# Performance work log

Hardware: AMD Instinct MI355X
Metric: run time of the kernel (lower is better)

## Reference

```python
import jax, jax.numpy as jnp
import numpy as np

E = 16          # num_expert
CAP = 1024


def setup_inputs() -> dict:
    key = jax.random.key(0)
    k1, k2, k3, k4 = jax.random.split(key, 4)
    B, L, D_in, D_out, S = 2, 4096, 1024, 4096, 512
    inp = jax.random.normal(k1, (B, L, D_in), jnp.float32)
    # counts must sum to B*L; use a balanced assignment (tokens pre-sorted by expert)
    fwd_expert_count = jnp.full((E,), (B * L) // E, dtype=jnp.int32)
    weight = jax.random.normal(k2, (E, D_out, D_in), jnp.float32) * (1.0 / np.sqrt(D_in))
    bias = jax.random.normal(k3, (E, D_out), jnp.float32) * 0.02
    components = jax.random.normal(k4, (E, S, D_out), jnp.float32) * (1.0 / np.sqrt(D_out))
    return {"inp": inp, "fwd_expert_count": fwd_expert_count, "weight": weight,
            "bias": bias, "components": components}


def _forward(inp, fwd_expert_count, weight, bias, components):
    flat = inp.reshape(-1, inp.shape[-1])            # [T, D_in]
    T = flat.shape[0]
    n_exp = fwd_expert_count.shape[0]
    counts = fwd_expert_count.astype(jnp.int32)
    # per-token expert id and position within its expert segment (tokens are
    # contiguous per expert, matching fastmoe's dispatch layout)
    expert_ids = jnp.repeat(jnp.arange(n_exp, dtype=jnp.int32), counts,
                            total_repeat_length=T)                    # [T]
    offsets = jnp.concatenate([jnp.zeros((1,), jnp.int32), jnp.cumsum(counts)])
    pos = jnp.arange(T, dtype=jnp.int32) - offsets[expert_ids]        # [T]
    # scatter tokens into a padded [E, CAP, D_in] buffer (static capacity)
    padded = jnp.zeros((n_exp, CAP, flat.shape[-1]), flat.dtype)
    padded = padded.at[expert_ids, pos].set(flat)
    # grouped expert GEMM: y_e = x_e @ W_e^T + b_e  (padded rows never read back)
    y = jnp.einsum('eci,eoi->eco', padded, weight) + bias[:, None, :]  # [E, CAP, D_out]
    # projection onto components (einsum 'nkd,ksd->nks' in padded layout)
    proj = jnp.einsum('ecd,esd->ecs', y, components)                   # [E, CAP, S]
    # gather real tokens back (the upscale_proj branch in the source is dead code:
    # its result is never used in the returned output)
    out = proj[expert_ids, pos]                                        # [T, S]
    return out.reshape(inp.shape[:-1] + (proj.shape[-1],))


def reference(inp, fwd_expert_count, weight, bias, components):
    return _forward(inp, fwd_expert_count, weight, bias, components)
```

## Files before the change

### kernel.cpp

```cpp
#include <hip/hip_runtime.h>


#define NEXP 16
#define TTOK 8192
#define DIN  1024
#define DOUT 4096
#define SDIM 512
#define LDSS 40

typedef short short8 __attribute__((ext_vector_type(8)));
typedef float floatx4 __attribute__((ext_vector_type(4)));
typedef unsigned short ushort_t;

__device__ __forceinline__ ushort_t f2bf(float f) {
    union { float f; unsigned u; } v; v.f = f;
    unsigned r = v.u + 0x7FFFu + ((v.u >> 16) & 1u);
    return (ushort_t)(r >> 16);
}

#define GLL16(g, l) __builtin_amdgcn_global_load_lds( \
    (const __attribute__((address_space(1))) void*)(g), \
    (__attribute__((address_space(3))) void*)(l), 16, 0, 0)

__global__ __launch_bounds__(256)
void cvt_kernel(const float* __restrict__ src, ushort_t* __restrict__ dst, int n8) {
    const int i = blockIdx.x * 256 + threadIdx.x;
    if (i >= n8) return;
    const float4 a = ((const float4*)src)[2 * i];
    const float4 b = ((const float4*)src)[2 * i + 1];
    short8 o;
    o[0] = (short)f2bf(a.x); o[1] = (short)f2bf(a.y);
    o[2] = (short)f2bf(a.z); o[3] = (short)f2bf(a.w);
    o[4] = (short)f2bf(b.x); o[5] = (short)f2bf(b.y);
    o[6] = (short)f2bf(b.z); o[7] = (short)f2bf(b.w);
    ((short8*)dst)[i] = o;
}

__global__ __launch_bounds__(256, 3)
void gemm1_f(const ushort_t* __restrict__ Xb, const int* __restrict__ counts,
             const ushort_t* __restrict__ Wb, const float* __restrict__ bias,
             ushort_t* __restrict__ Y) {
    __shared__ __align__(16) ushort_t As[128 * 32];
    __shared__ __align__(16) ushort_t Bs[128 * 32];

    const int l = ((blockIdx.x & 7) << 8) | (blockIdx.x >> 3);
    const int e = l >> 7;
    const int r = l & 127;
    const int n_tile = r >> 2, m_tile = r & 3;

    int off = 0;
    for (int i = 0; i < e; ++i) off += counts[i];
    const int cnt = counts[e];

    const int t = threadIdx.x, wave = t >> 6, lane = t & 63;
    const int wm = (wave & 1) << 6, wn = (wave >> 1) << 6;
    const int l15 = lane & 15, quad = lane >> 4;

    const int g = (lane & 3) ^ ((lane >> 3) & 3);
    const int c0 = wave * 2, c1 = wave * 2 + 1;
    const int ar0 = c0 * 16 + (lane >> 2), ar1 = c1 * 16 + (lane >> 2);
    int xr0 = off + (m_tile << 7) + ar0; if (xr0 >= TTOK) xr0 = TTOK - 1;
    int xr1 = off + (m_tile << 7) + ar1; if (xr1 >= TTOK) xr1 = TTOK - 1;
    const ushort_t* gA0 = Xb + (size_t)xr0 * DIN + g * 8;
    const ushort_t* gA1 = Xb + (size_t)xr1 * DIN + g * 8;
    const ushort_t* Wp = Wb + (size_t)e * DOUT * DIN + (size_t)(n_tile << 7) * DIN;
    const ushort_t* gB0 = Wp + (size_t)ar0 * DIN + g * 8;
    const ushort_t* gB1 = Wp + (size_t)ar1 * DIN + g * 8;
    ushort_t* lA0 = As + c0 * 512; ushort_t* lA1 = As + c1 * 512;
    ushort_t* lB0 = Bs + c0 * 512; ushort_t* lB1 = Bs + c1 * 512;

    const int sw = (quad ^ ((l15 >> 1) & 3)) << 3;

    floatx4 acc[4][4] = {};

    for (int k0 = 0; k0 < DIN; k0 += 32) {
        GLL16(gA0, lA0); GLL16(gA1, lA1);
        GLL16(gB0, lB0); GLL16(gB1, lB1);
        gA0 += 32; gA1 += 32; gB0 += 32; gB1 += 32;
        __syncthreads();
        short8 af[4], bfr[4];
        #pragma unroll
        for (int i = 0; i < 4; ++i) {
            af[i]  = *(const short8*)&As[(wm + (i << 4) + l15) * 32 + sw];
            bfr[i] = *(const short8*)&Bs[(wn + (i << 4) + l15) * 32 + sw];
        }
        #pragma unroll
        for (int mi = 0; mi < 4; ++mi)
            #pragma unroll
            for (int ni = 0; ni < 4; ++ni)
                acc[mi][ni] = __builtin_amdgcn_mfma_f32_16x16x32_bf16(
                    af[mi], bfr[ni], acc[mi][ni], 0, 0, 0);
        __syncthreads();
    }

    float bv[4];
    #pragma unroll
    for (int ni = 0; ni < 4; ++ni)
        bv[ni] = bias[e * DOUT + (n_tile << 7) + wn + (ni << 4) + l15];

    #pragma unroll
    for (int mi = 0; mi < 4; ++mi) {
        #pragma unroll
        for (int rg = 0; rg < 4; ++rg) {
            const int trow = (m_tile << 7) + wm + (mi << 4) + (quad << 2) + rg;
            if (trow < cnt) {
                ushort_t* yp = Y + (size_t)(off + trow) * DOUT + (n_tile << 7) + wn;
                #pragma unroll
                for (int ni = 0; ni < 4; ++ni)
                    yp[(ni << 4) + l15] = f2bf(acc[mi][ni][rg] + bv[ni]);
            }
        }
    }
}

__global__ __launch_bounds__(256, 3)
void gemm2_f(const ushort_t* __restrict__ Y, const int* __restrict__ counts,
             const ushort_t* __restrict__ Cb, float* __restrict__ P) {
    __shared__ __align__(16) ushort_t As[128 * 32];
    __shared__ __align__(16) ushort_t Bs[128 * 32];

    const int l = ((blockIdx.x & 7) << 6) | (blockIdx.x >> 3);
    const int e = l >> 5;
    const int r = l & 31;
    const int n_tile = r >> 3;
    const int kh = (r >> 2) & 1;
    const int m_tile = r & 3;

    int off = 0;
    for (int i = 0; i < e; ++i) off += counts[i];
    const int cnt = counts[e];

    const int t = threadIdx.x, wave = t >> 6, lane = t & 63;
    const int wm = (wave & 1) << 6, wn = (wave >> 1) << 6;
    const int l15 = lane & 15, quad = lane >> 4;

    const int g = (lane & 3) ^ ((lane >> 3) & 3);
    const int c0 = wave * 2, c1 = wave * 2 + 1;
    const int ar0 = c0 * 16 + (lane >> 2), ar1 = c1 * 16 + (lane >> 2);
    int yr0 = off + (m_tile << 7) + ar0; if (yr0 >= TTOK) yr0 = TTOK - 1;
    int yr1 = off + (m_tile << 7) + ar1; if (yr1 >= TTOK) yr1 = TTOK - 1;
    const int kbase = kh * 2048;
    const ushort_t* gA0 = Y + (size_t)yr0 * DOUT + kbase + g * 8;
    const ushort_t* gA1 = Y + (size_t)yr1 * DOUT + kbase + g * 8;
    const ushort_t* Cp = Cb + (size_t)e * SDIM * DOUT + (size_t)(n_tile << 7) * DOUT;
    const ushort_t* gB0 = Cp + (size_t)ar0 * DOUT + kbase + g * 8;
    const ushort_t* gB1 = Cp + (size_t)ar1 * DOUT + kbase + g * 8;
    ushort_t* lA0 = As + c0 * 512; ushort_t* lA1 = As + c1 * 512;
    ushort_t* lB0 = Bs + c0 * 512; ushort_t* lB1 = Bs + c1 * 512;

    const int sw = (quad ^ ((l15 >> 1) & 3)) << 3;

    floatx4 acc[4][4] = {};

    for (int it = 0; it < 64; ++it) {
        GLL16(gA0, lA0); GLL16(gA1, lA1);
        GLL16(gB0, lB0); GLL16(gB1, lB1);
        gA0 += 32; gA1 += 32; gB0 += 32; gB1 += 32;
        __syncthreads();
        short8 af[4], bfr[4];
        #pragma unroll
        for (int i = 0; i < 4; ++i) {
            af[i]  = *(const short8*)&As[(wm + (i << 4) + l15) * 32 + sw];
            bfr[i] = *(const short8*)&Bs[(wn + (i << 4) + l15) * 32 + sw];
        }
        #pragma unroll
        for (int mi = 0; mi < 4; ++mi)
            #pragma unroll
            for (int ni = 0; ni < 4; ++ni)
                acc[mi][ni] = __builtin_amdgcn_mfma_f32_16x16x32_bf16(
                    af[mi], bfr[ni], acc[mi][ni], 0, 0, 0);
        __syncthreads();
    }

    float* Pk = P + (size_t)kh * (TTOK * SDIM);
    #pragma unroll
    for (int mi = 0; mi < 4; ++mi) {
        #pragma unroll
        for (int rg = 0; rg < 4; ++rg) {
            const int trow = (m_tile << 7) + wm + (mi << 4) + (quad << 2) + rg;
            if (trow < cnt) {
                float* op = Pk + (size_t)(off + trow) * SDIM + (n_tile << 7) + wn;
                #pragma unroll
                for (int ni = 0; ni < 4; ++ni)
                    op[(ni << 4) + l15] = acc[mi][ni][rg];
            }
        }
    }
}

__global__ __launch_bounds__(256)
void reduce2_kernel(const float* __restrict__ P, float* __restrict__ O) {
    const int i = blockIdx.x * 256 + threadIdx.x;
    const float4 a = ((const float4*)P)[i];
    const float4 b = ((const float4*)(P + (size_t)TTOK * SDIM))[i];
    ((float4*)O)[i] = make_float4(a.x + b.x, a.y + b.y, a.z + b.z, a.w + b.w);
}

__global__ __launch_bounds__(256, 2)
void gemm1_o(const float* __restrict__ X, const int* __restrict__ counts,
             const float* __restrict__ W, const float* __restrict__ bias,
             ushort_t* __restrict__ Y) {
    __shared__ __align__(16) ushort_t As[128 * LDSS];
    __shared__ __align__(16) ushort_t Bs[128 * LDSS];
    const int bid = blockIdx.x;
    const int e = bid >> 7, r_ = bid & 127;
    const int n_tile = r_ >> 2, m_tile = r_ & 3;
    int off = 0;
    for (int i = 0; i < e; ++i) off += counts[i];
    const int cnt = counts[e];
    const int t = threadIdx.x, wave = t >> 6, lane = t & 63;
    const int wm = (wave & 1) << 6, wn = (wave >> 1) << 6;
    const int l15 = lane & 15, quad = lane >> 4;
    const float* Wp = W + (size_t)e * DOUT * DIN + (size_t)(n_tile << 7) * DIN;
    floatx4 acc[4][4] = {};
    const int srow = t >> 3, scol = (t & 7) << 2;
    for (int k0 = 0; k0 < DIN; k0 += 32) {
        #pragma unroll
        for (int p = 0; p < 4; ++p) {
            const int row = srow + (p << 5);
            int grow = off + (m_tile << 7) + row;
            if (grow >= TTOK) grow = 0;
            const float4 v = *(const float4*)(X + (size_t)grow * DIN + k0 + scol);
            unsigned lo = (unsigned)f2bf(v.x) | ((unsigned)f2bf(v.y) << 16);
            unsigned hi = (unsigned)f2bf(v.z) | ((unsigned)f2bf(v.w) << 16);
            *(uint2*)&As[row * LDSS + scol] = make_uint2(lo, hi);
        }
        #pragma unroll
        for (int p = 0; p < 4; ++p) {
            const int row = srow + (p << 5);
            const float4 v = *(const float4*)(Wp + (size_t)row * DIN + k0 + scol);
            unsigned lo = (unsigned)f2bf(v.x) | ((unsigned)f2bf(v.y) << 16);
            unsigned hi = (unsigned)f2bf(v.z) | ((unsigned)f2bf(v.w) << 16);
            *(uint2*)&Bs[row * LDSS + scol] = make_uint2(lo, hi);
        }
        __syncthreads();
        short8 af[4], bfr[4];
        #pragma unroll
        for (int i = 0; i < 4; ++i) {
            af[i]  = *(const short8*)&As[(wm + (i << 4) + l15) * LDSS + (quad << 3)];
            bfr[i] = *(const short8*)&Bs[(wn + (i << 4) + l15) * LDSS + (quad << 3)];
        }
        #pragma unroll
        for (int mi = 0; mi < 4; ++mi)
            #pragma unroll
            for (int ni = 0; ni < 4; ++ni)
                acc[mi][ni] = __builtin_amdgcn_mfma_f32_16x16x32_bf16(
                    af[mi], bfr[ni], acc[mi][ni], 0, 0, 0);
        __syncthreads();
    }
    float bv[4];
    #pragma unroll
    for (int ni = 0; ni < 4; ++ni)
        bv[ni] = bias[e * DOUT + (n_tile << 7) + wn + (ni << 4) + l15];
    #pragma unroll
    for (int mi = 0; mi < 4; ++mi)
        #pragma unroll
        for (int rg = 0; rg < 4; ++rg) {
            const int trow = (m_tile << 7) + wm + (mi << 4) + (quad << 2) + rg;
            if (trow < cnt) {
                ushort_t* yp = Y + (size_t)(off + trow) * DOUT + (n_tile << 7) + wn;
                #pragma unroll
                for (int ni = 0; ni < 4; ++ni)
                    yp[(ni << 4) + l15] = f2bf(acc[mi][ni][rg] + bv[ni]);
            }
        }
}

__global__ __launch_bounds__(256, 2)
void gemm2_o(const ushort_t* __restrict__ Y, const int* __restrict__ counts,
             const float* __restrict__ C, float* __restrict__ O) {
    __shared__ __align__(16) ushort_t As[128 * LDSS];
    __shared__ __align__(16) ushort_t Bs[128 * LDSS];
    const int bid = blockIdx.x;
    const int e = bid >> 4, r_ = bid & 15;
    const int n_tile = r_ >> 2, m_tile = r_ & 3;
    int off = 0;
    for (int i = 0; i < e; ++i) off += counts[i];
    const int cnt = counts[e];
    const int t = threadIdx.x, wave = t >> 6, lane = t & 63;
    const int wm = (wave & 1) << 6, wn = (wave >> 1) << 6;
    const int l15 = lane & 15, quad = lane >> 4;
    const float* Cp = C + (size_t)e * SDIM * DOUT + (size_t)(n_tile << 7) * DOUT;
    floatx4 acc[4][4] = {};
    const int arow = t >> 2, achk = (t & 3) << 3;
    const int srow = t >> 3, scol = (t & 7) << 2;
    for (int k0 = 0; k0 < DOUT; k0 += 32) {
        #pragma unroll
        for (int p = 0; p < 2; ++p) {
            const int row = arow + (p << 6);
            int grow = off + (m_tile << 7) + row;
            if (grow >= TTOK) grow = 0;
            const short8 v = *(const short8*)(Y + (size_t)grow * DOUT + k0 + achk);
            *(short8*)&As[row * LDSS + achk] = v;
        }
        #pragma unroll
        for (int p = 0; p < 4; ++p) {
            const int row = srow + (p << 5);
            const float4 v = *(const float4*)(Cp + (size_t)row * DOUT + k0 + scol);
            unsigned lo = (unsigned)f2bf(v.x) | ((unsigned)f2bf(v.y) << 16);
            unsigned hi = (unsigned)f2bf(v.z) | ((unsigned)f2bf(v.w) << 16);
            *(uint2*)&Bs[row * LDSS + scol] = make_uint2(lo, hi);
        }
        __syncthreads();
        short8 af[4], bfr[4];
        #pragma unroll
        for (int i = 0; i < 4; ++i) {
            af[i]  = *(const short8*)&As[(wm + (i << 4) + l15) * LDSS + (quad << 3)];
            bfr[i] = *(const short8*)&Bs[(wn + (i << 4) + l15) * LDSS + (quad << 3)];
        }
        #pragma unroll
        for (int mi = 0; mi < 4; ++mi)
            #pragma unroll
            for (int ni = 0; ni < 4; ++ni)
                acc[mi][ni] = __builtin_amdgcn_mfma_f32_16x16x32_bf16(
                    af[mi], bfr[ni], acc[mi][ni], 0, 0, 0);
        __syncthreads();
    }
    #pragma unroll
    for (int mi = 0; mi < 4; ++mi)
        #pragma unroll
        for (int rg = 0; rg < 4; ++rg) {
            const int trow = (m_tile << 7) + wm + (mi << 4) + (quad << 2) + rg;
            if (trow < cnt) {
                float* op = O + (size_t)(off + trow) * SDIM + (n_tile << 7) + wn;
                #pragma unroll
                for (int ni = 0; ni < 4; ++ni)
                    op[(ni << 4) + l15] = acc[mi][ni][rg];
            }
        }
}

extern "C" void kernel_launch(void* const* d_in, const int* in_sizes, int n_in,
                              void* d_out, int out_size, void* d_ws, size_t ws_size,
                              hipStream_t stream) {
    const float* X      = (const float*)d_in[0];
    const int*   counts = (const int*)d_in[1];
    const float* W      = (const float*)d_in[2];
    const float* bias   = (const float*)d_in[3];
    const float* comp   = (const float*)d_in[4];
    float* out = (float*)d_out;

    const size_t OFF_XB = 0;
    const size_t OFF_WB = 16777216;
    const size_t OFF_CB = 150994944;
    const size_t OFF_Y  = 218103808;
    const size_t NEED   = 285212672;

    if (ws_size >= NEED) {
        ushort_t* Xb = (ushort_t*)((char*)d_ws + OFF_XB);
        ushort_t* Wb = (ushort_t*)((char*)d_ws + OFF_WB);
        ushort_t* Cb = (ushort_t*)((char*)d_ws + OFF_CB);
        ushort_t* Y  = (ushort_t*)((char*)d_ws + OFF_Y);
        float*    P  = (float*)d_ws;

        cvt_kernel<<<dim3(4096),  dim3(256), 0, stream>>>(X, Xb, 1048576);
        cvt_kernel<<<dim3(32768), dim3(256), 0, stream>>>(W, Wb, 8388608);
        cvt_kernel<<<dim3(16384), dim3(256), 0, stream>>>(comp, Cb, 4194304);
        gemm1_f<<<dim3(2048), dim3(256), 0, stream>>>(Xb, counts, Wb, bias, Y);
        gemm2_f<<<dim3(512),  dim3(256), 0, stream>>>(Y, counts, Cb, P);
        reduce2_kernel<<<dim3(4096), dim3(256), 0, stream>>>(P, out);
    } else {
        ushort_t* Y = (ushort_t*)d_ws;
        gemm1_o<<<dim3(2048), dim3(256), 0, stream>>>(X, counts, W, bias, Y);
        gemm2_o<<<dim3(256),  dim3(256), 0, stream>>>(Y, counts, comp, out);
    }
}
```

Before: 654.6 us.

## Replace bf16 GEMMs with 256x256-tile double-buffered 8-wave pipelined kernel

Replaces the two 128x128, 4-wave, single-buffered grouped GEMMs with one templated 512-thread kernel. It uses 256x256 tiles, BK=64 double-buffered LDS, XOR-swizzled layout and interleaved global_load_lds prefetch with manual vmcnt waits and MFMA priority boosts. The second GEMM now splits K four ways instead of two, and a 4-way reduce kernel sums the partials. P is moved to the weight-bf16 region so it doesn't overlap Xb. The intent is more data reuse per tile and overlap of loads with MFMA. The cost is larger LDS use (128KB per block) and more partial-sum traffic.

```diff
diff --git a/kernel.cpp b/kernel.cpp
--- a/kernel.cpp
+++ b/kernel.cpp
@@ -36,164 +36,177 @@
     ((short8*)dst)[i] = o;
 }
 
-__global__ __launch_bounds__(256, 3)
-void gemm1_f(const ushort_t* __restrict__ Xb, const int* __restrict__ counts,
-             const ushort_t* __restrict__ Wb, const float* __restrict__ bias,
-             ushort_t* __restrict__ Y) {
-    __shared__ __align__(16) ushort_t As[128 * 32];
-    __shared__ __align__(16) ushort_t Bs[128 * 32];
-
-    const int l = ((blockIdx.x & 7) << 8) | (blockIdx.x >> 3);
-    const int e = l >> 7;
-    const int r = l & 127;
-    const int n_tile = r >> 2, m_tile = r & 3;
+template<bool G1>
+__global__ __launch_bounds__(512, 2)
+void gemm8p(const ushort_t* __restrict__ Ain, const int* __restrict__ counts,
+            const ushort_t* __restrict__ Bin, const float* __restrict__ bias,
+            ushort_t* __restrict__ Yout, float* __restrict__ Pout) {
+    __shared__ __align__(16) ushort_t As[2 * 16384];
+    __shared__ __align__(16) ushort_t Bs[2 * 16384];
+
+    int e, mt, nt, kq;
+    if constexpr (G1) {
+        const int l = ((blockIdx.x & 7) << 6) | (blockIdx.x >> 3);
+        e = l >> 5; nt = (l >> 1) & 15; mt = l & 1; kq = 0;
+    } else {
+        const int l = ((blockIdx.x & 7) << 5) | (blockIdx.x >> 3);
+        e = l >> 4; kq = (l >> 2) & 3; nt = (l >> 1) & 1; mt = l & 1;
+    }
+    const int LDK = G1 ? DIN : DOUT;
 
     int off = 0;
     for (int i = 0; i < e; ++i) off += counts[i];
     const int cnt = counts[e];
 
-    const int t = threadIdx.x, wave = t >> 6, lane = t & 63;
-    const int wm = (wave & 1) << 6, wn = (wave >> 1) << 6;
+    const int tid = threadIdx.x, wave = tid >> 6, lane = tid & 63;
+    const int wm = wave >> 2, wn = wave & 3;
     const int l15 = lane & 15, quad = lane >> 4;
 
-    const int g = (lane & 3) ^ ((lane >> 3) & 3);
-    const int c0 = wave * 2, c1 = wave * 2 + 1;
-    const int ar0 = c0 * 16 + (lane >> 2), ar1 = c1 * 16 + (lane >> 2);
-    int xr0 = off + (m_tile << 7) + ar0; if (xr0 >= TTOK) xr0 = TTOK - 1;
-    int xr1 = off + (m_tile << 7) + ar1; if (xr1 >= TTOK) xr1 = TTOK - 1;
-    const ushort_t* gA0 = Xb + (size_t)xr0 * DIN + g * 8;
-    const ushort_t* gA1 = Xb + (size_t)xr1 * DIN + g * 8;
-    const ushort_t* Wp = Wb + (size_t)e * DOUT * DIN + (size_t)(n_tile << 7) * DIN;
-    const ushort_t* gB0 = Wp + (size_t)ar0 * DIN + g * 8;
-    const ushort_t* gB1 = Wp + (size_t)ar1 * DIN + g * 8;
-    ushort_t* lA0 = As + c0 * 512; ushort_t* lA1 = As + c1 * 512;
-    ushort_t* lB0 = Bs + c0 * 512; ushort_t* lB1 = Bs + c1 * 512;
-
-    const int sw = (quad ^ ((l15 >> 1) & 3)) << 3;
-
-    floatx4 acc[4][4] = {};
-
-    for (int k0 = 0; k0 < DIN; k0 += 32) {
-        GLL16(gA0, lA0); GLL16(gA1, lA1);
-        GLL16(gB0, lB0); GLL16(gB1, lB1);
-        gA0 += 32; gA1 += 32; gB0 += 32; gB1 += 32;
-        __syncthreads();
-        short8 af[4], bfr[4];
-        #pragma unroll
-        for (int i = 0; i < 4; ++i) {
-            af[i]  = *(const short8*)&As[(wm + (i << 4) + l15) * 32 + sw];
-            bfr[i] = *(const short8*)&Bs[(wn + (i << 4) + l15) * 32 + sw];
-        }
-        #pragma unroll
-        for (int mi = 0; mi < 4; ++mi)
+    const int srow  = (wave << 3) + (lane >> 3);
+    const int kbase = (G1 ? 0 : (kq << 10)) + (((lane & 7) ^ (lane >> 3)) << 3);
+
+    const ushort_t* Bseg;
+    if constexpr (G1) Bseg = Bin + (size_t)e * DOUT * DIN  + ((size_t)(nt << 8)) * DIN;
+    else              Bseg = Bin + (size_t)e * SDIM * DOUT + ((size_t)(nt << 8)) * DOUT;
+    const int aseg = off + (mt << 8);
+
+    auto stA = [&](int bufe, int q, int kt) {
+        int r = aseg + (q << 6) + srow; if (r >= TTOK) r = TTOK - 1;
+        GLL16(Ain + (size_t)r * LDK + kbase + (kt << 6),
+              As + bufe + (q << 12) + (wave << 9));
+    };
+    auto stB = [&](int bufe, int q, int kt) {
+        GLL16(Bseg + (size_t)((q << 6) + srow) * LDK + kbase + (kt << 6),
+              Bs + bufe + (q << 12) + (wave << 9));
+    };
+    auto rdA = [&](int bufe, int m, int s) -> short8 {
+        return *(const short8*)&As[bufe + ((wm << 7) + (m << 4) + l15) * 64
+                                   + ((((s << 2) | quad) ^ (lane & 7)) << 3)];
+    };
+    auto rdB = [&](int bufe, int n, int s) -> short8 {
+        return *(const short8*)&Bs[bufe + ((wn << 6) + (n << 4) + l15) * 64
+                                   + ((((s << 2) | quad) ^ (lane & 7)) << 3)];
+    };
+
+    floatx4 acc[8][4] = {};
+    short8 bf[4][2], af0[2], af1[2];
+
+#define RDB_ALL(BUFE) { _Pragma("unroll") \
+    for (int n = 0; n < 4; ++n) { bf[n][0] = rdB(BUFE,n,0); bf[n][1] = rdB(BUFE,n,1); } }
+#define RDA2(BUFE, M0) { af0[0]=rdA(BUFE,M0,0); af0[1]=rdA(BUFE,M0,1); \
+                         af1[0]=rdA(BUFE,(M0)+1,0); af1[1]=rdA(BUFE,(M0)+1,1); }
+#define MFMA16(M0) { \
+    __builtin_amdgcn_s_setprio(1); \
+    _Pragma("unroll") for (int n = 0; n < 4; ++n) { \
+      acc[M0][n]     = __builtin_amdgcn_mfma_f32_16x16x32_bf16(af0[0], bf[n][0], acc[M0][n],     0,0,0); \
+      acc[M0][n]     = __builtin_amdgcn_mfma_f32_16x16x32_bf16(af0[1], bf[n][1], acc[M0][n],     0,0,0); \
+      acc[(M0)+1][n] = __builtin_amdgcn_mfma_f32_16x16x32_bf16(af1[0], bf[n][0], acc[(M0)+1][n], 0,0,0); \
+      acc[(M0)+1][n] = __builtin_amdgcn_mfma_f32_16x16x32_bf16(af1[1], bf[n][1], acc[(M0)+1][n], 0,0,0); } \
+    __builtin_amdgcn_s_setprio(0); }
+#define BAR() __builtin_amdgcn_s_barrier()
+#define VMC6() asm volatile("s_waitcnt vmcnt(6)" ::: "memory")
+
+    stA(0,0,0); stA(0,1,0); stA(0,2,0); stA(0,3,0);
+    stB(0,0,0); stB(0,1,0); stB(0,2,0); stB(0,3,0);
+    stB(16384,0,1); stB(16384,1,1); stB(16384,2,1); stB(16384,3,1);
+    stA(16384,0,1); stA(16384,2,1);
+    VMC6();
+    BAR();
+
+    #pragma unroll 1
+    for (int it = 0; it < 8; ++it) {
+        const int tn = 2 * it + 1;
+        const int t2 = (it < 7) ? 2 * it + 2 : 0;
+        const int t3 = (it < 7) ? 2 * it + 3 : 1;
+
+        RDB_ALL(0); RDA2(0, 0);
+        stA(16384,1,tn); stA(16384,3,tn);
+        BAR(); MFMA16(0); BAR();
+
+        RDA2(0, 2);
+        stB(0,0,t2); stB(0,1,t2);
+        BAR(); MFMA16(2); BAR();
+
+        RDA2(0, 4);
+        stB(0,2,t2); stA(0,0,t2);
+        BAR(); MFMA16(4); BAR();
+
+        RDA2(0, 6);
+        stB(0,3,t2); stA(0,2,t2);
+        VMC6();
+        BAR(); MFMA16(6); BAR();
+
+        RDB_ALL(16384); RDA2(16384, 0);
+        stA(0,1,t2); stA(0,3,t2);
+        BAR(); MFMA16(0); BAR();
+
+        RDA2(16384, 2);
+        stB(16384,0,t3); stB(16384,1,t3);
+        BAR(); MFMA16(2); BAR();
+
+        RDA2(16384, 4);
+        stB(16384,2,t3); stA(16384,0,t3);
+        BAR(); MFMA16(4); BAR();
+
+        RDA2(16384, 6);
+        stB(16384,3,t3); stA(16384,2,t3);
+        VMC6();
+        BAR(); MFMA16(6); BAR();
+    }
+    asm volatile("s_waitcnt vmcnt(0)" ::: "memory");
+
+#undef RDB_ALL
+#undef RDA2
+#undef MFMA16
+#undef BAR
+#undef VMC6
+
+    if constexpr (G1) {
+        float bv[4];
+        #pragma unroll
+        for (int n = 0; n < 4; ++n)
+            bv[n] = bias[e * DOUT + (nt << 8) + (wn << 6) + (n << 4) + l15];
+        #pragma unroll
+        for (int m = 0; m < 8; ++m) {
             #pragma unroll
-            for (int ni = 0; ni < 4; ++ni)
-                acc[mi][ni] = __builtin_amdgcn_mfma_f32_16x16x32_bf16(
-                    af[mi], bfr[ni], acc[mi][ni], 0, 0, 0);
-        __syncthreads();
-    }
-
-    float bv[4];
-    #pragma unroll
-    for (int ni = 0; ni < 4; ++ni)
-        bv[ni] = bias[e * DOUT + (n_tile << 7) + wn + (ni << 4) + l15];
-
-    #pragma unroll
-    for (int mi = 0; mi < 4; ++mi) {
-        #pragma unroll
-        for (int rg = 0; rg < 4; ++rg) {
-            const int trow = (m_tile << 7) + wm + (mi << 4) + (quad << 2) + rg;
-            if (trow < cnt) {
-                ushort_t* yp = Y + (size_t)(off + trow) * DOUT + (n_tile << 7) + wn;
-                #pragma unroll
-                for (int ni = 0; ni < 4; ++ni)
-                    yp[(ni << 4) + l15] = f2bf(acc[mi][ni][rg] + bv[ni]);
+            for (int rg = 0; rg < 4; ++rg) {
+                const int trow = (mt << 8) + (wm << 7) + (m << 4) + (quad << 2) + rg;
+                if (trow < cnt) {
+                    ushort_t* yp = Yout + (size_t)(off + trow) * DOUT + (nt << 8) + (wn << 6);
+                    #pragma unroll
+                    for (int n = 0; n < 4; ++n)
+                        yp[(n << 4) + l15] = f2bf(acc[m][n][rg] + bv[n]);
+                }
             }
         }
-    }
-}
-
-__global__ __launch_bounds__(256, 3)
-void gemm2_f(const ushort_t* __restrict__ Y, const int* __restrict__ counts,
-             const ushort_t* __restrict__ Cb, float* __restrict__ P) {
-    __shared__ __align__(16) ushort_t As[128 * 32];
-    __shared__ __align__(16) ushort_t Bs[128 * 32];
-
-    const int l = ((blockIdx.x & 7) << 6) | (blockIdx.x >> 3);
-    const int e = l >> 5;
-    const int r = l & 31;
-    const int n_tile = r >> 3;
-    const int kh = (r >> 2) & 1;
-    const int m_tile = r & 3;
-
-    int off = 0;
-    for (int i = 0; i < e; ++i) off += counts[i];
-    const int cnt = counts[e];
-
-    const int t = threadIdx.x, wave = t >> 6, lane = t & 63;
-    const int wm = (wave & 1) << 6, wn = (wave >> 1) << 6;
-    const int l15 = lane & 15, quad = lane >> 4;
-
-    const int g = (lane & 3) ^ ((lane >> 3) & 3);
-    const int c0 = wave * 2, c1 = wave * 2 + 1;
-    const int ar0 = c0 * 16 + (lane >> 2), ar1 = c1 * 16 + (lane >> 2);
-    int yr0 = off + (m_tile << 7) + ar0; if (yr0 >= TTOK) yr0 = TTOK - 1;
-    int yr1 = off + (m_tile << 7) + ar1; if (yr1 >= TTOK) yr1 = TTOK - 1;
-    const int kbase = kh * 2048;
-    const ushort_t* gA0 = Y + (size_t)yr0 * DOUT + kbase + g * 8;
-    const ushort_t* gA1 = Y + (size_t)yr1 * DOUT + kbase + g * 8;
-    const ushort_t* Cp = Cb + (size_t)e * SDIM * DOUT + (size_t)(n_tile << 7) * DOUT;
-    const ushort_t* gB0 = Cp + (size_t)ar0 * DOUT + kbase + g * 8;
-    const ushort_t* gB1 = Cp + (size_t)ar1 * DOUT + kbase + g * 8;
-    ushort_t* lA0 = As + c0 * 512; ushort_t* lA1 = As + c1 * 512;
-    ushort_t* lB0 = Bs + c0 * 512; ushort_t* lB1 = Bs + c1 * 512;
-
-    const int sw = (quad ^ ((l15 >> 1) & 3)) << 3;
-
-    floatx4 acc[4][4] = {};
-
-    for (int it = 0; it < 64; ++it) {
-        GLL16(gA0, lA0); GLL16(gA1, lA1);
-        GLL16(gB0, lB0); GLL16(gB1, lB1);
-        gA0 += 32; gA1 += 32; gB0 += 32; gB1 += 32;
-        __syncthreads();
-        short8 af[4], bfr[4];
-        #pragma unroll
-        for (int i = 0; i < 4; ++i) {
-            af[i]  = *(const short8*)&As[(wm + (i << 4) + l15) * 32 + sw];
-            bfr[i] = *(const short8*)&Bs[(wn + (i << 4) + l15) * 32 + sw];
-        }
-        #pragma unroll
-        for (int mi = 0; mi < 4; ++mi)
+    } else {
+        float* pp = Pout + (size_t)kq * ((size_t)TTOK * SDIM);
+        #pragma unroll
+        for (int m = 0; m < 8; ++m) {
             #pragma unroll
-            for (int ni = 0; ni < 4; ++ni)
-                acc[mi][ni] = __builtin_amdgcn_mfma_f32_16x16x32_bf16(
-                    af[mi], bfr[ni], acc[mi][ni], 0, 0, 0);
-        __syncthreads();
-    }
-
-    float* Pk = P + (size_t)kh * (TTOK * SDIM);
-    #pragma unroll
-    for (int mi = 0; mi < 4; ++mi) {
-        #pragma unroll
-        for (int rg = 0; rg < 4; ++rg) {
-            const int trow = (m_tile << 7) + wm + (mi << 4) + (quad << 2) + rg;
-            if (trow < cnt) {
-                float* op = Pk + (size_t)(off + trow) * SDIM + (n_tile << 7) + wn;
-                #pragma unroll
-                for (int ni = 0; ni < 4; ++ni)
-                    op[(ni << 4) + l15] = acc[mi][ni][rg];
+            for (int rg = 0; rg < 4; ++rg) {
+                const int trow = (mt << 8) + (wm << 7) + (m << 4) + (quad << 2) + rg;
+                if (trow < cnt) {
+                    float* op = pp + (size_t)(off + trow) * SDIM + (nt << 8) + (wn << 6);
+                    #pragma unroll
+                    for (int n = 0; n < 4; ++n)
+                        op[(n << 4) + l15] = acc[m][n][rg];
+                }
             }
         }
     }
 }
 
 __global__ __launch_bounds__(256)
-void reduce2_kernel(const float* __restrict__ P, float* __restrict__ O) {
+void reduce4_kernel(const float* __restrict__ P, float* __restrict__ O) {
     const int i = blockIdx.x * 256 + threadIdx.x;
+    const size_t S = (size_t)TTOK * SDIM;
     const float4 a = ((const float4*)P)[i];
-    const float4 b = ((const float4*)(P + (size_t)TTOK * SDIM))[i];
-    ((float4*)O)[i] = make_float4(a.x + b.x, a.y + b.y, a.z + b.z, a.w + b.w);
+    const float4 b = ((const float4*)(P + S))[i];
+    const float4 c = ((const float4*)(P + 2 * S))[i];
+    const float4 d = ((const float4*)(P + 3 * S))[i];
+    ((float4*)O)[i] = make_float4(a.x + b.x + c.x + d.x, a.y + b.y + c.y + d.y,
+                                  a.z + b.z + c.z + d.z, a.w + b.w + c.w + d.w);
 }
 
 __global__ __launch_bounds__(256, 2)
@@ -351,14 +364,14 @@
         ushort_t* Wb = (ushort_t*)((char*)d_ws + OFF_WB);
         ushort_t* Cb = (ushort_t*)((char*)d_ws + OFF_CB);
         ushort_t* Y  = (ushort_t*)((char*)d_ws + OFF_Y);
-        float*    P  = (float*)d_ws;
+        float*    P  = (float*)((char*)d_ws + OFF_WB);
 
         cvt_kernel<<<dim3(4096),  dim3(256), 0, stream>>>(X, Xb, 1048576);
         cvt_kernel<<<dim3(32768), dim3(256), 0, stream>>>(W, Wb, 8388608);
         cvt_kernel<<<dim3(16384), dim3(256), 0, stream>>>(comp, Cb, 4194304);
-        gemm1_f<<<dim3(2048), dim3(256), 0, stream>>>(Xb, counts, Wb, bias, Y);
-        gemm2_f<<<dim3(512),  dim3(256), 0, stream>>>(Y, counts, Cb, P);
-        reduce2_kernel<<<dim3(4096), dim3(256), 0, stream>>>(P, out);
+        gemm8p<true><<<dim3(512),  dim3(512), 0, stream>>>(Xb, counts, Wb, bias, Y, nullptr);
+        gemm8p<false><<<dim3(256), dim3(512), 0, stream>>>(Y, counts, Cb, nullptr, nullptr, P);
+        reduce4_kernel<<<dim3(4096), dim3(256), 0, stream>>>(P, out);
     } else {
         ushort_t* Y = (ushort_t*)d_ws;
         gemm1_o<<<dim3(2048), dim3(256), 0, stream>>>(X, counts, W, bias, Y);
```

Measured after the change: 633.2 us. 1.03x faster.
